# Optimization experiments

Measured on AMD Instinct MI355X. Metric: run time of the kernel, lower is better.

The kernel has to match this reference:

```python
import jax, jax.numpy as jnp
import numpy as np

NUM_LEVELS = 256
SIGMA = 0.5


def _soft_bins(x, centers):
    # x: (b,c,h,w) -> (b,c,h,w,num_levels)
    return jnp.exp(-(x[..., None] - centers) ** 2 / (2.0 * SIGMA ** 2))


def _shift0(b, d):
    r = jnp.roll(b, -d, axis=3)
    return r.at[:, :, :, -d:, :].set(0.0)


def _shift45(b, d):
    r = jnp.roll(b, (d, -d), axis=(2, 3))
    r = r.at[:, :, :d, :, :].set(0.0)
    return r.at[:, :, :, -d:, :].set(0.0)


def _shift90(b, d):
    r = jnp.roll(b, d, axis=2)
    return r.at[:, :, :d, :, :].set(0.0)


def _shift135(b, d):
    r = jnp.roll(b, (d, d), axis=(2, 3))
    r = r.at[:, :, :d, :, :].set(0.0)
    return r.at[:, :, :, :d, :].set(0.0)


def _glcm_contrast(bins, shifted, weights):
    # co-occurrence: reduce spatial dims into (b,c,j,k)
    occ = jnp.einsum('bchwj,bchwk->bcjk', bins, shifted)
    g = occ + jnp.swapaxes(occ, 2, 3)
    s = jnp.sum(g, axis=(2, 3), keepdims=True)
    s = jnp.where(s == 0, jnp.ones_like(s), s)
    g = g / s
    # Haralick contrast
    return jnp.sum(g * weights, axis=(2, 3))  # (b,c)


def _extract_grid(x):
    idx = jnp.arange(NUM_LEVELS, dtype=jnp.float32)
    weights = ((idx[:, None] - idx[None, :]) ** 2)[None, None, :, :]  # (1,1,L,L)

    centers_a = jnp.linspace(-1.0, 1.0, NUM_LEVELS)   # theta 0/45 use max_r=1
    centers_b = jnp.linspace(-1.0, -1.0, NUM_LEVELS)  # theta 90/135 use max_r=-1 (as in source)

    bins_a = _soft_bins(x, centers_a)  # (b,c,h,w,L)
    bins_b = _soft_bins(x, centers_b)

    grid = []
    for d in [1, 3, 5, 7]:
        grid.append(_glcm_contrast(bins_a, _shift0(bins_a, d), weights))
    for d in [1, 2, 4, 6]:
        grid.append(_glcm_contrast(bins_a, _shift45(bins_a, d), weights))
    for d in [1, 3, 5, 7]:
        grid.append(_glcm_contrast(bins_b, _shift90(bins_b, d), weights))
    for d in [1, 2, 4, 6]:
        grid.append(_glcm_contrast(bins_b, _shift135(bins_b, d), weights))

    return jnp.concatenate(grid, axis=0).reshape(x.shape[0], 1, 4, 4)


def setup_inputs() -> dict:
    key = jax.random.key(0)
    x = jax.random.normal(key, (4, 1, 256, 256), dtype=jnp.float32)
    return {"x": x}


def reference(x):
    return _extract_grid(x)
```

## Files before the change

kernel.cpp:

```cpp
#include <hip/hip_runtime.h>

#define HH 256
#define WW 256
#define NPIX (HH*WW)
#define NBATCH 4
#define TOTPIX (NPIX*NBATCH)
#define RPB 2
#define NBX (HH/RPB)
#define NPAIR 32

__global__ __launch_bounds__(256) void moments_kernel(
        const float* __restrict__ x, float4* __restrict__ m) {
    int i = blockIdx.x * 256 + threadIdx.x;
    float xv = x[i];

    const float h    = 1.0f / 255.0f;
    const float invS = 127.5f;
    const float K    = 0.626657068658f;
    const float SQ2  = 1.41421356237f;

    float u1 = (1.0f + h) - xv;
    float u0 = (-1.0f - h) - xv;
    float A  = SQ2 * u1;
    float B  = SQ2 * u0;

    float I0 = K * (erff(A) - erff(B));
    float eA = __expf(-A * A);
    float eB = __expf(-B * B);
    float I1 = 0.25f * (eB - eA);
    float I2 = 0.25f * (u0 * eB - u1 * eA) + 0.25f * I0;

    float S0  = invS * I0;
    float Sc  = invS * fmaf(xv, I0, I1);
    float Scc = invS * (xv * xv * I0 + 2.0f * xv * I1 + I2);

    float s0 = S0;
    float s1 = invS * (Sc + S0);
    float s2 = invS * invS * (Scc + 2.0f * Sc + S0);

    m[i] = make_float4(s0, s1, s2, 0.0f);
}

__global__ __launch_bounds__(256) void glcm_kernel(
        const float4* __restrict__ m, float* __restrict__ part) {
    const int batch = blockIdx.y;
    const int w     = threadIdx.x;
    const int r0    = blockIdx.x * RPB;
    const float4* mb = m + batch * NPIX;

    float num[8] = {0,0,0,0,0,0,0,0};
    float den[8] = {0,0,0,0,0,0,0,0};
    const int d0[4]  = {1,3,5,7};
    const int d45[4] = {1,2,4,6};

    #pragma unroll
    for (int rr = 0; rr < RPB; ++rr) {
        int r   = r0 + rr;
        int idx = r * WW + w;
        float4 P = mb[idx];
        #pragma unroll
        for (int k = 0; k < 4; ++k) {
            int d = d0[k];
            if (w < WW - d) {
                float4 Q = mb[idx + d];
                den[k] = fmaf(P.x, Q.x, den[k]);
                num[k] = fmaf(P.z, Q.x, num[k]);
                num[k] = fmaf(P.x, Q.z, num[k]);
                num[k] = fmaf(-2.0f * P.y, Q.y, num[k]);
            }
        }
        #pragma unroll
        for (int k = 0; k < 4; ++k) {
            int d = d45[k];
            if (r >= d && w < WW - d) {
                float4 Q = mb[idx + d - d * WW];
                den[k+4] = fmaf(P.x, Q.x, den[k+4]);
                num[k+4] = fmaf(P.z, Q.x, num[k+4]);
                num[k+4] = fmaf(P.x, Q.z, num[k+4]);
                num[k+4] = fmaf(-2.0f * P.y, Q.y, num[k+4]);
            }
        }
    }

    #pragma unroll
    for (int off = 32; off > 0; off >>= 1) {
        #pragma unroll
        for (int k = 0; k < 8; ++k) {
            num[k] += __shfl_down(num[k], off);
            den[k] += __shfl_down(den[k], off);
        }
    }
    __shared__ float sred[4][16];
    int lane = threadIdx.x & 63, wave = threadIdx.x >> 6;
    if (lane == 0) {
        #pragma unroll
        for (int k = 0; k < 8; ++k) {
            sred[wave][k]     = num[k];
            sred[wave][k + 8] = den[k];
        }
    }
    __syncthreads();
    if (threadIdx.x < 16) {
        int k = threadIdx.x;
        float v = sred[0][k] + sred[1][k] + sred[2][k] + sred[3][k];
        if (k < 8) {
            int pair = k * 4 + batch;
            part[pair * NBX + blockIdx.x] = v;
        } else {
            int pair = (k - 8) * 4 + batch;
            part[NPAIR * NBX + pair * NBX + blockIdx.x] = v;
        }
    }
}

__global__ void finalize_kernel(const float* __restrict__ part, float* __restrict__ out) {
    int n = threadIdx.x;
    int c = n >> 2;
    float v;
    if (c < 8) {
        float num = 0.f, den = 0.f;
        for (int b = 0; b < NBX; ++b) {
            num += part[n * NBX + b];
            den += part[NPAIR * NBX + n * NBX + b];
        }
        v = num / den;
    } else {
        v = 715816960.0 / 65536.0;
    }
    out[n] = v;
}

extern "C" void kernel_launch(void* const* d_in, const int* in_sizes, int n_in,
                              void* d_out, int out_size, void* d_ws, size_t ws_size,
                              hipStream_t stream) {
    const float* x = (const float*)d_in[0];
    float* out = (float*)d_out;

    float4* m   = (float4*)d_ws;
    float* part = (float*)d_ws + TOTPIX * 4;

    moments_kernel<<<TOTPIX / 256, 256, 0, stream>>>(x, m);

    dim3 grid2(NBX, NBATCH);
    glcm_kernel<<<grid2, 256, 0, stream>>>(m, part);

    finalize_kernel<<<1, 64, 0, stream>>>(part, out);
}
```

Measured before the change: 66.28 us.

## Fuse moments computation into GLCM kernel with shared-memory halo rows

The separate moments kernel, which wrote a float4 per pixel to global memory, is removed. Each GLCM block now computes the moments for its rows plus a 6-row halo directly into LDS and reads its neighbours from there. This drops one launch and the global round-trip of the moment buffer. In exchange, halo rows get their erf/exp work recomputed by neighbouring blocks, with 2.5x redundancy at RPB=4. The finalize kernel is also spread across 256 threads with a shuffle reduction.

```diff
diff --git a/kernel.cpp b/kernel.cpp
--- a/kernel.cpp
+++ b/kernel.cpp
@@ -4,16 +4,13 @@
 #define WW 256
 #define NPIX (HH*WW)
 #define NBATCH 4
-#define TOTPIX (NPIX*NBATCH)
-#define RPB 2
+#define RPB 4
+#define HALO 6
+#define LROWS (RPB+HALO)
 #define NBX (HH/RPB)
 #define NPAIR 32
 
-__global__ __launch_bounds__(256) void moments_kernel(
-        const float* __restrict__ x, float4* __restrict__ m) {
-    int i = blockIdx.x * 256 + threadIdx.x;
-    float xv = x[i];
-
+__device__ __forceinline__ void moments(float xv, float& s0, float& s1, float& s2) {
     const float h    = 1.0f / 255.0f;
     const float invS = 127.5f;
     const float K    = 0.626657068658f;
@@ -34,50 +31,63 @@
     float Sc  = invS * fmaf(xv, I0, I1);
     float Scc = invS * (xv * xv * I0 + 2.0f * xv * I1 + I2);
 
-    float s0 = S0;
-    float s1 = invS * (Sc + S0);
-    float s2 = invS * invS * (Scc + 2.0f * Sc + S0);
-
-    m[i] = make_float4(s0, s1, s2, 0.0f);
+    s0 = S0;
+    s1 = invS * (Sc + S0);
+    s2 = invS * invS * (Scc + 2.0f * Sc + S0);
 }
 
-__global__ __launch_bounds__(256) void glcm_kernel(
-        const float4* __restrict__ m, float* __restrict__ part) {
+__global__ __launch_bounds__(256) void fused_kernel(const float* __restrict__ x,
+                                                    float* __restrict__ part) {
+    __shared__ float ls0[LROWS][WW];
+    __shared__ float ls1[LROWS][WW];
+    __shared__ float ls2[LROWS][WW];
+    __shared__ float sred[4][16];
+
+    const int w     = threadIdx.x;
+    const int bx    = blockIdx.x;
     const int batch = blockIdx.y;
-    const int w     = threadIdx.x;
-    const int r0    = blockIdx.x * RPB;
-    const float4* mb = m + batch * NPIX;
+    const int r0    = bx * RPB;
+    const float* xb = x + batch * NPIX;
 
+    #pragma unroll
+    for (int i = 0; i < LROWS; ++i) {
+        int g = r0 - HALO + i;
+        float s0 = 0.f, s1 = 0.f, s2 = 0.f;
+        if (g >= 0) moments(xb[g * WW + w], s0, s1, s2);
+        ls0[i][w] = s0; ls1[i][w] = s1; ls2[i][w] = s2;
+    }
+    __syncthreads();
+
+    const int d0t[4]  = {1, 3, 5, 7};
+    const int d45t[4] = {1, 2, 4, 6};
     float num[8] = {0,0,0,0,0,0,0,0};
     float den[8] = {0,0,0,0,0,0,0,0};
-    const int d0[4]  = {1,3,5,7};
-    const int d45[4] = {1,2,4,6};
 
     #pragma unroll
     for (int rr = 0; rr < RPB; ++rr) {
-        int r   = r0 + rr;
-        int idx = r * WW + w;
-        float4 P = mb[idx];
+        int lr = rr + HALO;
+        int r  = r0 + rr;
+        float P0 = ls0[lr][w], P1 = ls1[lr][w], P2 = ls2[lr][w];
         #pragma unroll
         for (int k = 0; k < 4; ++k) {
-            int d = d0[k];
+            int d = d0t[k];
             if (w < WW - d) {
-                float4 Q = mb[idx + d];
-                den[k] = fmaf(P.x, Q.x, den[k]);
-                num[k] = fmaf(P.z, Q.x, num[k]);
-                num[k] = fmaf(P.x, Q.z, num[k]);
-                num[k] = fmaf(-2.0f * P.y, Q.y, num[k]);
+                float Q0 = ls0[lr][w + d], Q1 = ls1[lr][w + d], Q2 = ls2[lr][w + d];
+                den[k] = fmaf(P0, Q0, den[k]);
+                num[k] = fmaf(P2, Q0, num[k]);
+                num[k] = fmaf(P0, Q2, num[k]);
+                num[k] = fmaf(-2.0f * P1, Q1, num[k]);
             }
         }
         #pragma unroll
         for (int k = 0; k < 4; ++k) {
-            int d = d45[k];
+            int d = d45t[k];
             if (r >= d && w < WW - d) {
-                float4 Q = mb[idx + d - d * WW];
-                den[k+4] = fmaf(P.x, Q.x, den[k+4]);
-                num[k+4] = fmaf(P.z, Q.x, num[k+4]);
-                num[k+4] = fmaf(P.x, Q.z, num[k+4]);
-                num[k+4] = fmaf(-2.0f * P.y, Q.y, num[k+4]);
+                float Q0 = ls0[lr - d][w + d], Q1 = ls1[lr - d][w + d], Q2 = ls2[lr - d][w + d];
+                den[k + 4] = fmaf(P0, Q0, den[k + 4]);
+                num[k + 4] = fmaf(P2, Q0, num[k + 4]);
+                num[k + 4] = fmaf(P0, Q2, num[k + 4]);
+                num[k + 4] = fmaf(-2.0f * P1, Q1, num[k + 4]);
             }
         }
     }
@@ -90,44 +100,38 @@
             den[k] += __shfl_down(den[k], off);
         }
     }
-    __shared__ float sred[4][16];
     int lane = threadIdx.x & 63, wave = threadIdx.x >> 6;
     if (lane == 0) {
         #pragma unroll
-        for (int k = 0; k < 8; ++k) {
-            sred[wave][k]     = num[k];
-            sred[wave][k + 8] = den[k];
-        }
+        for (int k = 0; k < 8; ++k) { sred[wave][k] = num[k]; sred[wave][k + 8] = den[k]; }
     }
     __syncthreads();
     if (threadIdx.x < 16) {
         int k = threadIdx.x;
         float v = sred[0][k] + sred[1][k] + sred[2][k] + sred[3][k];
-        if (k < 8) {
-            int pair = k * 4 + batch;
-            part[pair * NBX + blockIdx.x] = v;
-        } else {
-            int pair = (k - 8) * 4 + batch;
-            part[NPAIR * NBX + pair * NBX + blockIdx.x] = v;
-        }
+        int pair = (k & 7) * 4 + batch;
+        int off  = (k < 8) ? 0 : NPAIR * NBX;
+        part[off + pair * NBX + bx] = v;
     }
 }
 
 __global__ void finalize_kernel(const float* __restrict__ part, float* __restrict__ out) {
-    int n = threadIdx.x;
-    int c = n >> 2;
-    float v;
-    if (c < 8) {
-        float num = 0.f, den = 0.f;
-        for (int b = 0; b < NBX; ++b) {
-            num += part[n * NBX + b];
-            den += part[NPAIR * NBX + n * NBX + b];
+    int t = threadIdx.x;
+    int p = t >> 2;
+    int c = t & 3;
+    float num = 0.f, den = 0.f;
+    if (p < NPAIR) {
+        #pragma unroll
+        for (int b = 0; b < 16; ++b) {
+            num += part[p * NBX + c * 16 + b];
+            den += part[NPAIR * NBX + p * NBX + c * 16 + b];
         }
-        v = num / den;
-    } else {
-        v = 715816960.0 / 65536.0;
     }
-    out[n] = v;
+    num += __shfl_down(num, 2); num += __shfl_down(num, 1);
+    den += __shfl_down(den, 2); den += __shfl_down(den, 1);
+    if (c == 0) {
+        out[p] = (p < NPAIR) ? (num / den) : (float)(715816960.0 / 65536.0);
+    }
 }
 
 extern "C" void kernel_launch(void* const* d_in, const int* in_sizes, int n_in,
@@ -135,14 +139,9 @@
                               hipStream_t stream) {
     const float* x = (const float*)d_in[0];
     float* out = (float*)d_out;
+    float* part = (float*)d_ws;
 
-    float4* m   = (float4*)d_ws;
-    float* part = (float*)d_ws + TOTPIX * 4;
-
-    moments_kernel<<<TOTPIX / 256, 256, 0, stream>>>(x, m);
-
-    dim3 grid2(NBX, NBATCH);
-    glcm_kernel<<<grid2, 256, 0, stream>>>(m, part);
-
-    finalize_kernel<<<1, 64, 0, stream>>>(part, out);
+    dim3 g1(NBX, NBATCH);
+    fused_kernel<<<g1, 256, 0, stream>>>(x, part);
+    finalize_kernel<<<1, 256, 0, stream>>>(part, out);
 }
```

Measured after the change: 62.39 us, median of 2. 1.06x faster.
